# Optimization experiments

Measured on AMD Instinct MI355X. Metric: run time of the kernel, lower is better.

## Reference

```python
import jax, jax.numpy as jnp
import numpy as np

N = 50000       # nodes
E = 800000      # edges
D = 64          # node_feats
H = 4           # heads
NEG_SLOPE = 0.2
LN_EPS = 1e-5


def setup_inputs() -> dict:
    key = jax.random.key(0)
    ks = jax.random.split(key, 8)
    h = jax.random.normal(ks[0], (N, D), dtype=jnp.float32)
    src = jax.random.randint(ks[1], (E,), 0, N, dtype=jnp.int32)
    dst = jax.random.randint(ks[2], (E,), 0, N, dtype=jnp.int32)
    # parameters (kaiming-uniform-ish scaling)
    W_node = jax.random.normal(ks[3], (D, H * D), dtype=jnp.float32) * (1.0 / np.sqrt(D))
    b_node = jnp.zeros((H * D,), dtype=jnp.float32)
    att = jax.random.normal(ks[4], (H, 2 * D), dtype=jnp.float32) * (1.0 / np.sqrt(2 * D))
    W_scale = jax.random.normal(ks[5], (H * D, D), dtype=jnp.float32) * (1.0 / np.sqrt(H * D))
    bias = jnp.zeros((D,), dtype=jnp.float32)
    ln_gamma = jnp.ones((D,), dtype=jnp.float32)
    ln_beta = jnp.zeros((D,), dtype=jnp.float32)
    return {"h": h, "src": src, "dst": dst, "W_node": W_node, "b_node": b_node,
            "att": att, "W_scale": W_scale, "bias": bias,
            "ln_gamma": ln_gamma, "ln_beta": ln_beta}


def reference(h, src, dst, W_node, b_node, att, W_scale, bias, ln_gamma, ln_beta):
    n, d = h.shape
    heads = att.shape[0]
    # node linear projection -> [N, H, D]
    wv = (h @ W_node + b_node).reshape(n, heads, d)
    u = wv[src]            # [E, H, D] source features (messages)
    v = wv[dst]            # [E, H, D] destination features
    a_u, a_v = att[:, :d], att[:, d:]
    # attention logit per edge/head: sum(cat(u,v) * a)
    logit = jnp.einsum('ehd,hd->eh', u, a_u) + jnp.einsum('ehd,hd->eh', v, a_v)
    logit = jax.nn.leaky_relu(logit, NEG_SLOPE)
    # segment softmax over incoming edges of each dst node
    smax = jax.ops.segment_max(logit, dst, num_segments=n)        # [N, H]
    smax = jnp.where(jnp.isfinite(smax), smax, 0.0)               # nodes w/o in-edges
    ex = jnp.exp(logit - smax[dst])                               # [E, H]
    denom = jax.ops.segment_sum(ex, dst, num_segments=n)          # [N, H]
    agg = jax.ops.segment_sum(ex[:, :, None] * u, dst, num_segments=n)  # [N, H, D]
    agg = agg / jnp.maximum(denom, 1e-16)[:, :, None]
    # scale back to node_feats, residual, layernorm, relu (dropout = eval identity)
    h_new = agg.reshape(n, heads * d) @ W_scale + bias
    x = h_new + h
    mu = jnp.mean(x, axis=-1, keepdims=True)
    var = jnp.var(x, axis=-1, keepdims=True)
    xn = (x - mu) * jax.lax.rsqrt(var + LN_EPS)
    return jax.nn.relu(xn * ln_gamma + ln_beta)
```

## Files before the change

### kernel.cpp

```cpp
#include <hip/hip_runtime.h>
#include <hip/hip_fp16.h>

#define N_NODES 50000
#define N_EDGES 800000
#define NEG_SLOPE 0.2f
#define LN_EPS 1e-5f
#define NB_SCAN 196
#define ALPHA_BLOCKS 1024
#define DEG_BLOCKS 3125

typedef _Float16 f16;
typedef f16 f16x4 __attribute__((ext_vector_type(4)));
typedef f16 f16x8 __attribute__((ext_vector_type(8)));
typedef float f32x4 __attribute__((ext_vector_type(4)));

__global__ __launch_bounds__(256) void k_pre(
    const float* __restrict__ Wn, const float* __restrict__ bn,
    const float* __restrict__ att, const float* __restrict__ Ws,
    const float* __restrict__ bias,
    float* __restrict__ qu, float* __restrict__ qv, float* __restrict__ cuv,
    f16* __restrict__ Mt16, float* __restrict__ cvec)
{
    const int b = blockIdx.x, t = threadIdx.x;
    if (b < 64) {
        int e = b * 256 + t;
        int hd = e >> 12, k = (e >> 6) & 63, c = e & 63;
        float s = 0.f;
        for (int j = 0; j < 64; ++j)
            s = fmaf(Wn[k * 256 + hd * 64 + j], Ws[(hd * 64 + j) * 64 + c], s);
        Mt16[c * 256 + hd * 64 + k] = (f16)s;
    } else if (b == 64) {
        int hd = t >> 6, k = t & 63;
        float su = 0.f, sv = 0.f;
        for (int j = 0; j < 64; ++j) {
            float w = Wn[k * 256 + hd * 64 + j];
            su = fmaf(w, att[hd * 128 + j], su);
            sv = fmaf(w, att[hd * 128 + 64 + j], sv);
        }
        qu[hd * 64 + k] = su;
        qv[hd * 64 + k] = sv;
        if (t < 8) {
            int hh = t & 3;
            const float* a = att + hh * 128 + (t >> 2) * 64;
            float s = 0.f;
            for (int j = 0; j < 64; ++j) s = fmaf(bn[hh * 64 + j], a[j], s);
            cuv[t] = s;
        }
    } else {
        if (t < 64) {
            float s = bias[t];
            for (int kk = 0; kk < 256; ++kk) s = fmaf(bn[kk], Ws[kk * 64 + t], s);
            cvec[t] = s;
        }
    }
}

__global__ __launch_bounds__(256) void k_front2(
    const float* __restrict__ h, const int* __restrict__ dst,
    const float* __restrict__ qu, const float* __restrict__ qv, const float* __restrict__ cuv,
    __half* __restrict__ h16, float* __restrict__ alpha_u, float* __restrict__ alpha_v,
    int* __restrict__ deg, int* __restrict__ rank)
{
    const int t = threadIdx.x;
    if (blockIdx.x >= ALPHA_BLOCKS) {
        int e = (blockIdx.x - ALPHA_BLOCKS) * 256 + t;
        if (e < N_EDGES) rank[e] = atomicAdd(&deg[dst[e]], 1);
        return;
    }
    const int lane = t & 63;
    const int wid = blockIdx.x * 4 + (t >> 6);
    const float qur0 = qu[lane], qur1 = qu[64 + lane], qur2 = qu[128 + lane], qur3 = qu[192 + lane];
    const float qvr0 = qv[lane], qvr1 = qv[64 + lane], qvr2 = qv[128 + lane], qvr3 = qv[192 + lane];
    const float4 cu = *(const float4*)cuv;
    const float4 cv = *(const float4*)(cuv + 4);
    for (int n = wid; n < N_NODES; n += ALPHA_BLOCKS * 4) {
        float hv = h[(size_t)n * 64 + lane];
        h16[(size_t)n * 64 + lane] = __float2half(hv);
        float pu0 = hv * qur0, pu1 = hv * qur1, pu2 = hv * qur2, pu3 = hv * qur3;
        float pv0 = hv * qvr0, pv1 = hv * qvr1, pv2 = hv * qvr2, pv3 = hv * qvr3;
#pragma unroll
        for (int off = 32; off; off >>= 1) {
            pu0 += __shfl_xor(pu0, off);
            pu1 += __shfl_xor(pu1, off);
            pu2 += __shfl_xor(pu2, off);
            pu3 += __shfl_xor(pu3, off);
            pv0 += __shfl_xor(pv0, off);
            pv1 += __shfl_xor(pv1, off);
            pv2 += __shfl_xor(pv2, off);
            pv3 += __shfl_xor(pv3, off);
        }
        if (lane == 0) {
            *(float4*)(alpha_u + n * 4) = make_float4(pu0 + cu.x, pu1 + cu.y, pu2 + cu.z, pu3 + cu.w);
            *(float4*)(alpha_v + n * 4) = make_float4(pv0 + cv.x, pv1 + cv.y, pv2 + cv.z, pv3 + cv.w);
        }
    }
}

__device__ __forceinline__ int wave_incl_scan(int x, int lane) {
#pragma unroll
    for (int off = 1; off < 64; off <<= 1) {
        int y = __shfl_up(x, off);
        if (lane >= off) x += y;
    }
    return x;
}

__global__ __launch_bounds__(256) void k_scan1(const int* __restrict__ deg,
                                               int* __restrict__ rowptr, int* __restrict__ bsum) {
    __shared__ int wsum[4];
    const int t = threadIdx.x, lane = t & 63, w = t >> 6;
    const int i = blockIdx.x * 256 + t;
    int x = (i < N_NODES) ? deg[i] : 0;
    int incl = wave_incl_scan(x, lane);
    if (lane == 63) wsum[w] = incl;
    __syncthreads();
    int pre = 0;
    for (int ww = 0; ww < w; ++ww) pre += wsum[ww];
    if (i < N_NODES) rowptr[i] = pre + incl - x;
    if (t == 255) bsum[blockIdx.x] = pre + incl;
}

__global__ __launch_bounds__(256) void k_scan2(const int* __restrict__ bsum, int* __restrict__ boff) {
    __shared__ int wsum[4];
    const int t = threadIdx.x, lane = t & 63, w = t >> 6;
    int x = (t < NB_SCAN) ? bsum[t] : 0;
    int incl = wave_incl_scan(x, lane);
    if (lane == 63) wsum[w] = incl;
    __syncthreads();
    int pre = 0;
    for (int ww = 0; ww < w; ++ww) pre += wsum[ww];
    if (t < NB_SCAN) boff[t] = pre + incl - x;
}

__global__ __launch_bounds__(256) void k_scan3(int* __restrict__ rowptr, const int* __restrict__ boff) {
    const int i = blockIdx.x * 256 + threadIdx.x;
    if (i < N_NODES) rowptr[i] += boff[blockIdx.x];
    if (i == 0) rowptr[N_NODES] = N_EDGES;
}

__global__ __launch_bounds__(256) void k_scatter(
    const int* __restrict__ src, const int* __restrict__ dst,
    const int* __restrict__ rowptr, const int* __restrict__ rank,
    const float* __restrict__ alpha_u, const float* __restrict__ alpha_v,
    int* __restrict__ csr_src, float* __restrict__ csr_w)
{
    int e = blockIdx.x * 256 + threadIdx.x;
    if (e >= N_EDGES) return;
    const int s = src[e], d = dst[e];
    const int pos = rowptr[d] + rank[e];
    csr_src[pos] = s;
    const float4 au = *(const float4*)(alpha_u + (size_t)s * 4);
    const float4 av = *(const float4*)(alpha_v + (size_t)d * 4);
    float l0 = au.x + av.x; l0 = l0 > 0.f ? l0 : NEG_SLOPE * l0;
    float l1 = au.y + av.y; l1 = l1 > 0.f ? l1 : NEG_SLOPE * l1;
    float l2 = au.z + av.z; l2 = l2 > 0.f ? l2 : NEG_SLOPE * l2;
    float l3 = au.w + av.w; l3 = l3 > 0.f ? l3 : NEG_SLOPE * l3;
    *(float4*)(csr_w + (size_t)pos * 4) =
        make_float4(__expf(l0), __expf(l1), __expf(l2), __expf(l3));
}

__global__ __launch_bounds__(256) void k_agg3(
    const int* __restrict__ rowptr, const int* __restrict__ csr_src,
    const float* __restrict__ csr_w, const __half* __restrict__ h16,
    f16* __restrict__ aggh16, int n0, int n1)
{
    const int lane = threadIdx.x & 63;
    const int wid = (blockIdx.x * 256 + threadIdx.x) >> 6;
    const int nwaves = (gridDim.x * 256) >> 6;
    for (int n = n0 + wid; n < n1; n += nwaves) {
        const int r0 = rowptr[n], r1 = rowptr[n + 1];
        float d0 = 0.f, d1 = 0.f, d2 = 0.f, d3 = 0.f;
        float a0 = 0.f, a1 = 0.f, a2 = 0.f, a3 = 0.f;
        const int rlast = r1 - 1;
        for (int j = r0; j < r1; j += 8) {
            int jdx[8], s[8];
#pragma unroll
            for (int i = 0; i < 8; ++i) {
                int jj = j + i;
                jdx[i] = jj < rlast ? jj : rlast;
                s[i] = __builtin_amdgcn_readfirstlane(csr_src[jdx[i]]);
            }
            float hv[8];
#pragma unroll
            for (int i = 0; i < 8; ++i)
                hv[i] = __half2float(h16[(size_t)s[i] * 64 + lane]);
            float4 w[8];
#pragma unroll
            for (int i = 0; i < 8; ++i)
                w[i] = *(const float4*)(csr_w + (size_t)jdx[i] * 4);
#pragma unroll
            for (int i = 0; i < 8; ++i) {
                const bool valid = (j + i < r1);
                float e0 = valid ? w[i].x : 0.f;
                float e1 = valid ? w[i].y : 0.f;
                float e2 = valid ? w[i].z : 0.f;
                float e3 = valid ? w[i].w : 0.f;
                d0 += e0; a0 = fmaf(e0, hv[i], a0);
                d1 += e1; a1 = fmaf(e1, hv[i], a1);
                d2 += e2; a2 = fmaf(e2, hv[i], a2);
                d3 += e3; a3 = fmaf(e3, hv[i], a3);
            }
        }
        const float i0 = 1.0f / fmaxf(d0, 1e-16f);
        const float i1 = 1.0f / fmaxf(d1, 1e-16f);
        const float i2 = 1.0f / fmaxf(d2, 1e-16f);
        const float i3 = 1.0f / fmaxf(d3, 1e-16f);
        f16* __restrict__ arow = aggh16 + (size_t)n * 256;
        arow[lane]       = (f16)(a0 * i0);
        arow[64 + lane]  = (f16)(a1 * i1);
        arow[128 + lane] = (f16)(a2 * i2);
        arow[192 + lane] = (f16)(a3 * i3);
    }
}

__global__ __launch_bounds__(256) void k_post_mfma(
    const f16* __restrict__ aggh16, const f16* __restrict__ Mt16,
    const float* __restrict__ cvec, const float* __restrict__ h,
    const float* __restrict__ gamma_, const float* __restrict__ beta_,
    float* __restrict__ out)
{
    __shared__ f16 Mlds[64 * 256];
    const int t = threadIdx.x;
    {
        const uint4* g = (const uint4*)Mt16;
        uint4* l = (uint4*)Mlds;
#pragma unroll
        for (int i = 0; i < 8; ++i) {
            int ch = i * 256 + t;
            l[ch ^ ((ch >> 5) & 7)] = g[ch];
        }
    }
    __syncthreads();
    const int lane = t & 63;
    const int l15 = lane & 15, lg = lane >> 4;
    float cv_r[4], ga_r[4], be_r[4];
#pragma unroll
    for (int ct = 0; ct < 4; ++ct) {
        int c = ct * 16 + l15;
        cv_r[ct] = cvec[c]; ga_r[ct] = gamma_[c]; be_r[ct] = beta_[c];
    }
    const int wid0 = (blockIdx.x * 256 + t) >> 6;
    const int nw = (gridDim.x * 256) >> 6;
    for (int blk = wid0; blk < N_NODES / 16; blk += nw) {
        f32x4 acc[4] = {{0.f,0.f,0.f,0.f},{0.f,0.f,0.f,0.f},{0.f,0.f,0.f,0.f},{0.f,0.f,0.f,0.f}};
        const f16* arow = aggh16 + (size_t)(blk * 16 + l15) * 256 + 4 * lg;
#pragma unroll
        for (int ks = 0; ks < 8; ++ks) {
            f16x4 alo = *(const f16x4*)(arow + ks * 32);
            f16x4 ahi = *(const f16x4*)(arow + ks * 32 + 16);
            f16x8 a;
            a[0]=alo[0]; a[1]=alo[1]; a[2]=alo[2]; a[3]=alo[3];
            a[4]=ahi[0]; a[5]=ahi[1]; a[6]=ahi[2]; a[7]=ahi[3];
#pragma unroll
            for (int ct = 0; ct < 4; ++ct) {
                const int c = ct * 16 + l15;
                const int sw = (c & 7) << 3;
                const int u0 = (c * 256 + ks * 32 + 4 * lg);
                f16x4 blo = *(const f16x4*)(Mlds + (u0 ^ sw));
                f16x4 bhi = *(const f16x4*)(Mlds + ((u0 + 16) ^ sw));
                f16x8 b;
                b[0]=blo[0]; b[1]=blo[1]; b[2]=blo[2]; b[3]=blo[3];
                b[4]=bhi[0]; b[5]=bhi[1]; b[6]=bhi[2]; b[7]=bhi[3];
                acc[ct] = __builtin_amdgcn_mfma_f32_16x16x32_f16(a, b, acc[ct], 0, 0, 0);
            }
        }
#pragma unroll
        for (int e = 0; e < 4; ++e) {
            const int gr = blk * 16 + 4 * lg + e;
            float x[4];
            float s = 0.f;
#pragma unroll
            for (int ct = 0; ct < 4; ++ct) {
                x[ct] = acc[ct][e] + cv_r[ct] + h[(size_t)gr * 64 + ct * 16 + l15];
                s += x[ct];
            }
            s += __shfl_xor(s, 1); s += __shfl_xor(s, 2);
            s += __shfl_xor(s, 4); s += __shfl_xor(s, 8);
            const float mu = s * (1.0f / 64.0f);
            float v = 0.f;
#pragma unroll
            for (int ct = 0; ct < 4; ++ct) { float d = x[ct] - mu; v = fmaf(d, d, v); }
            v += __shfl_xor(v, 1); v += __shfl_xor(v, 2);
            v += __shfl_xor(v, 4); v += __shfl_xor(v, 8);
            const float rinv = rsqrtf(v * (1.0f / 64.0f) + LN_EPS);
#pragma unroll
            for (int ct = 0; ct < 4; ++ct) {
                float xn = (x[ct] - mu) * rinv;
                out[(size_t)gr * 64 + ct * 16 + l15] = fmaxf(xn * ga_r[ct] + be_r[ct], 0.0f);
            }
        }
    }
}

extern "C" void kernel_launch(void* const* d_in, const int* in_sizes, int n_in,
                              void* d_out, int out_size, void* d_ws, size_t ws_size,
                              hipStream_t stream) {
    const float* h      = (const float*)d_in[0];
    const int*   src    = (const int*)d_in[1];
    const int*   dst    = (const int*)d_in[2];
    const float* Wn     = (const float*)d_in[3];
    const float* bn     = (const float*)d_in[4];
    const float* att    = (const float*)d_in[5];
    const float* Ws     = (const float*)d_in[6];
    const float* bias   = (const float*)d_in[7];
    const float* gamma_ = (const float*)d_in[8];
    const float* beta_  = (const float*)d_in[9];
    float* out = (float*)d_out;

    char* ws = (char*)d_ws;
    size_t off = 0;
    auto alloc = [&](size_t bytes) { void* p = ws + off; off = (off + bytes + 255) & ~(size_t)255; return p; };
    __half* h16    = (__half*)alloc((size_t)N_NODES * 64 * 2);
    f16*   aggh16  = (f16*)alloc((size_t)N_NODES * 256 * 2);
    float* alpha_u = (float*)alloc((size_t)N_NODES * 4 * 4);
    float* alpha_v = (float*)alloc((size_t)N_NODES * 4 * 4);
    int*   deg     = (int*)alloc((size_t)N_NODES * 4);
    int*   rowptr  = (int*)alloc((size_t)(N_NODES + 1) * 4);
    int*   rank    = (int*)alloc((size_t)N_EDGES * 4);
    int*   bsum    = (int*)alloc((size_t)NB_SCAN * 4);
    int*   boff    = (int*)alloc((size_t)NB_SCAN * 4);
    int*   csr_src = (int*)alloc((size_t)N_EDGES * 4);
    float* csr_w   = (float*)alloc((size_t)N_EDGES * 4 * 4);
    float* qu      = (float*)alloc(256 * 4);
    float* qv      = (float*)alloc(256 * 4);
    float* cuv     = (float*)alloc(8 * 4);
    f16*   Mt16    = (f16*)alloc(16384 * 2);
    float* cvec    = (float*)alloc(64 * 4);

    hipMemsetAsync(deg, 0, (size_t)N_NODES * 4, stream);

    k_pre<<<66, 256, 0, stream>>>(Wn, bn, att, Ws, bias, qu, qv, cuv, Mt16, cvec);
    k_front2<<<ALPHA_BLOCKS + DEG_BLOCKS, 256, 0, stream>>>(h, dst, qu, qv, cuv,
                                                            h16, alpha_u, alpha_v, deg, rank);
    k_scan1<<<NB_SCAN, 256, 0, stream>>>(deg, rowptr, bsum);
    k_scan2<<<1, 256, 0, stream>>>(bsum, boff);
    k_scan3<<<NB_SCAN, 256, 0, stream>>>(rowptr, boff);
    k_scatter<<<DEG_BLOCKS, 256, 0, stream>>>(src, dst, rowptr, rank, alpha_u, alpha_v,
                                              csr_src, csr_w);
    k_agg3<<<2048, 256, 0, stream>>>(rowptr, csr_src, csr_w, h16, aggh16, 0, N_NODES / 2);
    k_agg3<<<2048, 256, 0, stream>>>(rowptr, csr_src, csr_w, h16, aggh16, N_NODES / 2, N_NODES);
    k_post_mfma<<<782, 256, 0, stream>>>(aggh16, Mt16, cvec, h, gamma_, beta_, out);
}
```

Baseline: 255.8 us.

## Replace atomic-degree CSR build with two-level bucketed counting sort

Builds the dst-sorted CSR with a two-pass radix-style sort instead of global atomics per edge. Edges are first binned into 128-node buckets using per-block shared-memory histograms, a column scan and a base scan. A second per-bucket kernel then does a local histogram, scans it, writes rowptr, and scatters the edges with their attention weights. The aim is to remove contended global atomics and scattered writes, at the cost of more kernels and extra histogram buffers. The aggregation is also split into four launches instead of two.

```diff
diff --git a/kernel.cpp b/kernel.cpp
--- a/kernel.cpp
+++ b/kernel.cpp
@@ -5,9 +5,10 @@
 #define N_EDGES 800000
 #define NEG_SLOPE 0.2f
 #define LN_EPS 1e-5f
-#define NB_SCAN 196
 #define ALPHA_BLOCKS 1024
-#define DEG_BLOCKS 3125
+#define H1_BLOCKS 3125
+#define NB1 391
+#define NB1P 392
 
 typedef _Float16 f16;
 typedef f16 f16x4 __attribute__((ext_vector_type(4)));
@@ -55,16 +56,22 @@
     }
 }
 
-__global__ __launch_bounds__(256) void k_front2(
+__global__ __launch_bounds__(256) void k_front3(
     const float* __restrict__ h, const int* __restrict__ dst,
     const float* __restrict__ qu, const float* __restrict__ qv, const float* __restrict__ cuv,
     __half* __restrict__ h16, float* __restrict__ alpha_u, float* __restrict__ alpha_v,
-    int* __restrict__ deg, int* __restrict__ rank)
-{
+    int* __restrict__ g)
+{
+    __shared__ int hist[NB1P];
     const int t = threadIdx.x;
     if (blockIdx.x >= ALPHA_BLOCKS) {
-        int e = (blockIdx.x - ALPHA_BLOCKS) * 256 + t;
-        if (e < N_EDGES) rank[e] = atomicAdd(&deg[dst[e]], 1);
+        const int blk = blockIdx.x - ALPHA_BLOCKS;
+        for (int i = t; i < NB1P; i += 256) hist[i] = 0;
+        __syncthreads();
+        const int e = blk * 256 + t;
+        atomicAdd(&hist[dst[e] >> 7], 1);
+        __syncthreads();
+        for (int i = t; i < NB1P; i += 256) g[blk * NB1P + i] = hist[i];
         return;
     }
     const int lane = t & 63;
@@ -105,58 +112,94 @@
     return x;
 }
 
-__global__ __launch_bounds__(256) void k_scan1(const int* __restrict__ deg,
-                                               int* __restrict__ rowptr, int* __restrict__ bsum) {
-    __shared__ int wsum[4];
-    const int t = threadIdx.x, lane = t & 63, w = t >> 6;
-    const int i = blockIdx.x * 256 + t;
-    int x = (i < N_NODES) ? deg[i] : 0;
-    int incl = wave_incl_scan(x, lane);
-    if (lane == 63) wsum[w] = incl;
-    __syncthreads();
-    int pre = 0;
-    for (int ww = 0; ww < w; ++ww) pre += wsum[ww];
-    if (i < N_NODES) rowptr[i] = pre + incl - x;
-    if (t == 255) bsum[blockIdx.x] = pre + incl;
-}
-
-__global__ __launch_bounds__(256) void k_scan2(const int* __restrict__ bsum, int* __restrict__ boff) {
-    __shared__ int wsum[4];
-    const int t = threadIdx.x, lane = t & 63, w = t >> 6;
-    int x = (t < NB_SCAN) ? bsum[t] : 0;
-    int incl = wave_incl_scan(x, lane);
-    if (lane == 63) wsum[w] = incl;
-    __syncthreads();
-    int pre = 0;
-    for (int ww = 0; ww < w; ++ww) pre += wsum[ww];
-    if (t < NB_SCAN) boff[t] = pre + incl - x;
-}
-
-__global__ __launch_bounds__(256) void k_scan3(int* __restrict__ rowptr, const int* __restrict__ boff) {
-    const int i = blockIdx.x * 256 + threadIdx.x;
-    if (i < N_NODES) rowptr[i] += boff[blockIdx.x];
-    if (i == 0) rowptr[N_NODES] = N_EDGES;
-}
-
-__global__ __launch_bounds__(256) void k_scatter(
+__global__ __launch_bounds__(64) void k_s1(const int* __restrict__ g,
+                                           int* __restrict__ off1, int* __restrict__ tot) {
+    const int b = blockIdx.x;
+    const int lane = threadIdx.x;
+    int running = 0;
+    for (int c = 0; c < H1_BLOCKS; c += 64) {
+        const int blk = c + lane;
+        int v = (blk < H1_BLOCKS) ? g[blk * NB1P + b] : 0;
+        int incl = wave_incl_scan(v, lane);
+        if (blk < H1_BLOCKS) off1[blk * NB1P + b] = running + incl - v;
+        running += __shfl(incl, 63);
+    }
+    if (lane == 0) tot[b] = running;
+}
+
+__global__ __launch_bounds__(64) void k_base(const int* __restrict__ tot, int* __restrict__ base) {
+    const int lane = threadIdx.x;
+    int running = 0;
+    for (int c = 0; c < NB1P; c += 64) {
+        const int i = c + lane;
+        int v = (i < NB1) ? tot[i] : 0;
+        int incl = wave_incl_scan(v, lane);
+        if (i < NB1P) base[i] = running + incl - v;
+        running += __shfl(incl, 63);
+    }
+}
+
+__global__ __launch_bounds__(256) void k_h1scat(
     const int* __restrict__ src, const int* __restrict__ dst,
-    const int* __restrict__ rowptr, const int* __restrict__ rank,
+    const int* __restrict__ base, const int* __restrict__ off1,
+    int* __restrict__ ebuf)
+{
+    __shared__ int cur[NB1P];
+    const int t = threadIdx.x;
+    const int blk = blockIdx.x;
+    for (int i = t; i < NB1P; i += 256)
+        cur[i] = (i < NB1) ? base[i] + off1[blk * NB1P + i] : 0;
+    __syncthreads();
+    const int e = blk * 256 + t;
+    const int s = src[e], d = dst[e];
+    const int pos = atomicAdd(&cur[d >> 7], 1);
+    ebuf[pos] = (s << 7) | (d & 127);
+}
+
+__global__ __launch_bounds__(256) void k_h2(
+    const int* __restrict__ ebuf, const int* __restrict__ base,
     const float* __restrict__ alpha_u, const float* __restrict__ alpha_v,
-    int* __restrict__ csr_src, float* __restrict__ csr_w)
-{
-    int e = blockIdx.x * 256 + threadIdx.x;
-    if (e >= N_EDGES) return;
-    const int s = src[e], d = dst[e];
-    const int pos = rowptr[d] + rank[e];
-    csr_src[pos] = s;
-    const float4 au = *(const float4*)(alpha_u + (size_t)s * 4);
-    const float4 av = *(const float4*)(alpha_v + (size_t)d * 4);
-    float l0 = au.x + av.x; l0 = l0 > 0.f ? l0 : NEG_SLOPE * l0;
-    float l1 = au.y + av.y; l1 = l1 > 0.f ? l1 : NEG_SLOPE * l1;
-    float l2 = au.z + av.z; l2 = l2 > 0.f ? l2 : NEG_SLOPE * l2;
-    float l3 = au.w + av.w; l3 = l3 > 0.f ? l3 : NEG_SLOPE * l3;
-    *(float4*)(csr_w + (size_t)pos * 4) =
-        make_float4(__expf(l0), __expf(l1), __expf(l2), __expf(l3));
+    int* __restrict__ rowptr, int* __restrict__ csr_src, float* __restrict__ csr_w)
+{
+    __shared__ int hist[128], lscan[128], cur[128];
+    const int t = threadIdx.x;
+    const int b = blockIdx.x;
+    const int r0 = base[b], r1 = base[b + 1];
+    if (t < 128) hist[t] = 0;
+    __syncthreads();
+    for (int j = r0 + t; j < r1; j += 256) atomicAdd(&hist[ebuf[j] & 127], 1);
+    __syncthreads();
+    if (t < 64) {
+        int running = 0;
+        for (int c = 0; c < 128; c += 64) {
+            int v = hist[c + t];
+            int incl = wave_incl_scan(v, t);
+            lscan[c + t] = running + incl - v;
+            running += __shfl(incl, 63);
+        }
+    }
+    __syncthreads();
+    if (t < 128) {
+        const int n = b * 128 + t;
+        if (n <= N_NODES) rowptr[n] = r0 + lscan[t];
+        cur[t] = lscan[t];
+    }
+    __syncthreads();
+    for (int j = r0 + t; j < r1; j += 256) {
+        const int p = ebuf[j];
+        const int dl = p & 127, s = p >> 7;
+        const int pos = r0 + atomicAdd(&cur[dl], 1);
+        const int d = b * 128 + dl;
+        const float4 au = *(const float4*)(alpha_u + (size_t)s * 4);
+        const float4 av = *(const float4*)(alpha_v + (size_t)d * 4);
+        float l0 = au.x + av.x; l0 = l0 > 0.f ? l0 : NEG_SLOPE * l0;
+        float l1 = au.y + av.y; l1 = l1 > 0.f ? l1 : NEG_SLOPE * l1;
+        float l2 = au.z + av.z; l2 = l2 > 0.f ? l2 : NEG_SLOPE * l2;
+        float l3 = au.w + av.w; l3 = l3 > 0.f ? l3 : NEG_SLOPE * l3;
+        csr_src[pos] = s;
+        *(float4*)(csr_w + (size_t)pos * 4) =
+            make_float4(__expf(l0), __expf(l1), __expf(l2), __expf(l3));
+    }
 }
 
 __global__ __launch_bounds__(256) void k_agg3(
@@ -314,30 +357,30 @@
     f16*   aggh16  = (f16*)alloc((size_t)N_NODES * 256 * 2);
     float* alpha_u = (float*)alloc((size_t)N_NODES * 4 * 4);
     float* alpha_v = (float*)alloc((size_t)N_NODES * 4 * 4);
-    int*   deg     = (int*)alloc((size_t)N_NODES * 4);
     int*   rowptr  = (int*)alloc((size_t)(N_NODES + 1) * 4);
-    int*   rank    = (int*)alloc((size_t)N_EDGES * 4);
-    int*   bsum    = (int*)alloc((size_t)NB_SCAN * 4);
-    int*   boff    = (int*)alloc((size_t)NB_SCAN * 4);
     int*   csr_src = (int*)alloc((size_t)N_EDGES * 4);
     float* csr_w   = (float*)alloc((size_t)N_EDGES * 4 * 4);
+    int*   g       = (int*)alloc((size_t)H1_BLOCKS * NB1P * 4);
+    int*   off1    = (int*)alloc((size_t)H1_BLOCKS * NB1P * 4);
+    int*   tot     = (int*)alloc((size_t)NB1P * 4);
+    int*   base    = (int*)alloc((size_t)(NB1P + 1) * 4);
+    int*   ebuf    = (int*)alloc((size_t)N_EDGES * 4);
     float* qu      = (float*)alloc(256 * 4);
     float* qv      = (float*)alloc(256 * 4);
     float* cuv     = (float*)alloc(8 * 4);
     f16*   Mt16    = (f16*)alloc(16384 * 2);
     float* cvec    = (float*)alloc(64 * 4);
 
-    hipMemsetAsync(deg, 0, (size_t)N_NODES * 4, stream);
-
     k_pre<<<66, 256, 0, stream>>>(Wn, bn, att, Ws, bias, qu, qv, cuv, Mt16, cvec);
-    k_front2<<<ALPHA_BLOCKS + DEG_BLOCKS, 256, 0, stream>>>(h, dst, qu, qv, cuv,
-                                                            h16, alpha_u, alpha_v, deg, rank);
-    k_scan1<<<NB_SCAN, 256, 0, stream>>>(deg, rowptr, bsum);
-    k_scan2<<<1, 256, 0, stream>>>(bsum, boff);
-    k_scan3<<<NB_SCAN, 256, 0, stream>>>(rowptr, boff);
-    k_scatter<<<DEG_BLOCKS, 256, 0, stream>>>(src, dst, rowptr, rank, alpha_u, alpha_v,
-                                              csr_src, csr_w);
-    k_agg3<<<2048, 256, 0, stream>>>(rowptr, csr_src, csr_w, h16, aggh16, 0, N_NODES / 2);
-    k_agg3<<<2048, 256, 0, stream>>>(rowptr, csr_src, csr_w, h16, aggh16, N_NODES / 2, N_NODES);
+    k_front3<<<ALPHA_BLOCKS + H1_BLOCKS, 256, 0, stream>>>(h, dst, qu, qv, cuv,
+                                                           h16, alpha_u, alpha_v, g);
+    k_s1<<<NB1, 64, 0, stream>>>(g, off1, tot);
+    k_base<<<1, 64, 0, stream>>>(tot, base);
+    k_h1scat<<<H1_BLOCKS, 256, 0, stream>>>(src, dst, base, off1, ebuf);
+    k_h2<<<NB1, 256, 0, stream>>>(ebuf, base, alpha_u, alpha_v, rowptr, csr_src, csr_w);
+    k_agg3<<<2048, 256, 0, stream>>>(rowptr, csr_src, csr_w, h16, aggh16, 0, 12500);
+    k_agg3<<<2048, 256, 0, stream>>>(rowptr, csr_src, csr_w, h16, aggh16, 12500, 25000);
+    k_agg3<<<2048, 256, 0, stream>>>(rowptr, csr_src, csr_w, h16, aggh16, 25000, 37500);
+    k_agg3<<<2048, 256, 0, stream>>>(rowptr, csr_src, csr_w, h16, aggh16, 37500, N_NODES);
     k_post_mfma<<<782, 256, 0, stream>>>(aggh16, Mt16, cvec, h, gamma_, beta_, out);
 }
```

New measurement: 263.1 us. +2.9%, slower.
